# Optimization experiments

Hardware: AMD Instinct MI355X
Metric: run time of the kernel (lower is better)

Reference implementation:

```python
import jax, jax.numpy as jnp
import numpy as np

FS = 100.0
NPERSEG = 200
Q = 2
N_POINTS = 2
N_COEF = 2 * Q + 1          # bandstop doubles prototype order: len(a) = 2*Q + 1
EDGE = 3 * N_COEF           # scipy filtfilt default padlen = 3*max(len(a), len(b))

# ---- numpy filter design (== scipy.signal.butter(Q, [lo, hi], 'bandstop', fs=fs)) ----
def _butter_bandstop(N, low, high, fs):
    Wn = np.array([low, high]) / (fs / 2.0)
    fs2 = 2.0
    warped = 2.0 * fs2 * np.tan(np.pi * Wn / fs2)           # bilinear prewarp
    k = np.arange(1, N + 1)
    p = np.exp(1j * np.pi * (2 * k + N - 1) / (2 * N))      # analog Butterworth poles
    wo = np.sqrt(warped[0] * warped[1]); bw = warped[1] - warped[0]
    p_hp = (bw / 2.0) / p                                   # lp2bs_zpk
    p_bs = np.concatenate([p_hp + np.sqrt(p_hp ** 2 - wo ** 2), p_hp - np.sqrt(p_hp ** 2 - wo ** 2)])
    z_bs = np.concatenate([np.full(N, 1j * wo), np.full(N, -1j * wo)])
    k_bs = np.real(1.0 / np.prod(-p))
    fs2b = 2.0 * fs2                                        # bilinear_zpk
    z_z = (fs2b + z_bs) / (fs2b - z_bs)
    p_z = (fs2b + p_bs) / (fs2b - p_bs)
    k_z = k_bs * np.real(np.prod(fs2b - z_bs) / np.prod(fs2b - p_bs))
    b = np.real(k_z * np.poly(z_z)); a = np.real(np.poly(p_z))
    return b, a

def _lfilter_zi(b, a):
    n = len(a)
    A = np.zeros((n - 1, n - 1)); A[0, :] = -a[1:] / a[0]; A[1:, :-1] = np.eye(n - 2)
    B = b[1:] - a[1:] * b[0]
    return np.linalg.solve(np.eye(n - 1) - A.T, B)


def setup_inputs() -> dict:
    key = jax.random.key(0)
    B, T, H = 64, 3000, 256
    df = FS / NPERSEG
    f0 = np.arange(NPERSEG // 2 + 1) * df                   # welch freqs
    f0[0] = f0[1]; f0[-1] = f0[-2]
    col0, col1 = f0[:-1], f0[1:]
    freq_index = np.argsort(-col0, kind='stable')           # 'highest' strategy, descending
    high = float(col1[-1])
    lows = col0[freq_index[2:-1]]                           # 97 bandstop low edges
    bs, az, zs = [], [], []
    for lo in lows:
        b, a = _butter_bandstop(Q, float(lo), high, FS)
        bs.append(b); az.append(a); zs.append(_lfilter_zi(b, a))
    kx, kw1, kw2 = jax.random.split(key, 3)
    return {
        'x': jax.random.normal(kx, (B, T), jnp.float32),
        'b_all': jnp.asarray(np.stack(bs), jnp.float32),
        'a_all': jnp.asarray(np.stack(az), jnp.float32),
        'zi_all': jnp.asarray(np.stack(zs), jnp.float32),
        'W1': jax.random.normal(kw1, (T, H), jnp.float32) / np.sqrt(T),
        'b1': jnp.zeros((H,), jnp.float32),
        'w2': jax.random.normal(kw2, (H,), jnp.float32) / np.sqrt(H),
        'freq_index': jnp.asarray(freq_index, jnp.int32),
    }


# ---- batched zero-phase IIR filtering over the whole filter bank ----
def _lfilter(b, a, x, zi):
    # b, a: [F, n]; x: [F, B, T]; zi: [F, B, n-1]; direct-form II transposed
    b0 = b[:, 0][:, None]
    b_rest = b[:, 1:][:, None, :]
    a_rest = a[:, 1:][:, None, :]
    def step(z, xt):
        y = b0 * xt + z[..., 0]
        z_shift = jnp.concatenate([z[..., 1:], jnp.zeros_like(z[..., :1])], axis=-1)
        return z_shift + b_rest * xt[..., None] - a_rest * y[..., None], y
    _, ys = jax.lax.scan(step, zi, jnp.moveaxis(x, -1, 0))
    return jnp.moveaxis(ys, 0, -1)

def _filtfilt(b, a, zi, x):
    # odd extension by EDGE samples on both ends (scipy padtype='odd')
    left = 2.0 * x[..., :1] - jnp.flip(x[..., 1:EDGE + 1], -1)
    right = 2.0 * x[..., -1:] - jnp.flip(x[..., -EDGE - 1:-1], -1)
    ext = jnp.concatenate([left, x, right], -1)
    y = _lfilter(b, a, ext, zi[:, None, :] * ext[..., :1])
    y = jnp.flip(_lfilter(b, a, jnp.flip(y, -1), zi[:, None, :] * y[..., -1:]), -1)
    return y[..., EDGE:-EDGE]

def _fn(p, W1, b1, w2):
    # explained model: scalar score per sample (last axis is time/features)
    return jnp.tanh(p @ W1 + b1) @ w2


def reference(x, b_all, a_all, zi_all, W1, b1, w2, freq_index):
    F = b_all.shape[0]
    bs_out = _filtfilt(b_all, a_all, zi_all, jnp.broadcast_to(x, (F,) + x.shape))  # [97,B,T]
    # filter outputs in order: Identity, Identity, 97 bandstops, SpectralErase; x_all[0] = start point
    x_all = jnp.concatenate([x[None], x[None], x[None], bs_out, jnp.zeros_like(x)[None]], 0)  # [101,B,T]
    x_next, x_prev = x_all[1:], x_all[:-1]
    delta = x_prev - x_next                                   # x_i - x_i1 (path from x_i1 to x_i)
    alphas = jnp.linspace(0.0, 1.0, N_POINTS).astype(x.dtype)
    pts = x_next[None] + alphas[:, None, None, None] * delta[None]  # [n_points,100,B,T]
    g = jax.grad(lambda p: _fn(p, W1, b1, w2).sum())(pts)           # per-sample grads (fn is batched)
    grads = g.mean(0) * delta                                       # line integral, [100,B,T]
    out = jnp.moveaxis(grads, 0, -1)                                # [B,T,100]
    return out[:, :, freq_index]
```

## Files before the change

kernel.cpp:

```cpp
#include <hip/hip_runtime.h>
#include <math.h>

#define T_LEN 3000
#define NF 97
#define NB 64
#define NH 256
#define NI 100
#define SEQ 6336
#define KCO 16
#define KS 10
#define KPB 300
#define KC2 15
#define UPROWS 6400
#define LF 202
#define LB 201
#define NSEG 15
#define WTS 3072
#define VTS 6400

__device__ __forceinline__ void gload16(const float* g, float* l) {
    __builtin_amdgcn_global_load_lds(
        (const __attribute__((address_space(1))) void*)g,
        (__attribute__((address_space(3))) void*)l, 16, 0, 0);
}

__global__ __launch_bounds__(256) void k_prep(
    const float* __restrict__ x, float* __restrict__ Pt)
{
    const int kk0 = blockIdx.x * 64;
    const int b   = threadIdx.x & 63;
    const int ko  = threadIdx.x >> 6;
    #pragma unroll
    for (int p = 0; p < 16; ++p) {
        int kk = kk0 + ko + 4*p;
        if (kk < T_LEN) Pt[(size_t)kk*SEQ + b] = x[(size_t)b*T_LEN + kk];
    }
}

__global__ __launch_bounds__(256) void k_wt(
    const float* __restrict__ W1, float* __restrict__ W1T)
{
    __shared__ float tile[64][65];
    const int tb = blockIdx.x;
    const int hb = blockIdx.y;
    const int lt = threadIdx.x & 63, lw = threadIdx.x >> 6;
    #pragma unroll
    for (int i = 0; i < 16; ++i) {
        int t = tb*64 + lw*16 + i; if (t > T_LEN-1) t = T_LEN-1;
        tile[lw*16+i][lt] = W1[(size_t)t*NH + hb*64 + lt];
    }
    __syncthreads();
    #pragma unroll
    for (int i = 0; i < 16; ++i) {
        int h = hb*64 + lw*16 + i;
        W1T[(size_t)h*WTS + tb*64 + lt] = tile[lt][lw*16+i];
    }
}

__global__ __launch_bounds__(64) void k_hom(
    const float* __restrict__ a_all, double* __restrict__ H,
    double* __restrict__ Mbd, double* __restrict__ Mfd)
{
    const int ft = blockIdx.x*64 + threadIdx.x;
    const int f = ft >> 2, ib = ft & 3;
    if (f >= NF) return;
    const double a1 = a_all[f*5+1], a2 = a_all[f*5+2],
                 a3 = a_all[f*5+3], a4 = a_all[f*5+4];
    double z0 = (ib==0), z1 = (ib==1), z2 = (ib==2), z3 = (ib==3);
    for (int j = 0; j <= LF; ++j) {
        if (j < LF) H[((size_t)f*LF + j)*4 + ib] = z0;
        if (j == LB) {
            Mbd[f*16 + 0*4 + ib] = z0; Mbd[f*16 + 1*4 + ib] = z1;
            Mbd[f*16 + 2*4 + ib] = z2; Mbd[f*16 + 3*4 + ib] = z3;
        }
        if (j == LF) {
            Mfd[f*16 + 0*4 + ib] = z0; Mfd[f*16 + 1*4 + ib] = z1;
            Mfd[f*16 + 2*4 + ib] = z2; Mfd[f*16 + 3*4 + ib] = z3;
            break;
        }
        double yv = z0;
        z0 = z1 - a1*yv; z1 = z2 - a2*yv; z2 = z3 - a3*yv; z3 = -a4*yv;
    }
}

#define COEFS \
    const double bc0 = b_all[f*5+0], bc1 = b_all[f*5+1], bc2 = b_all[f*5+2], \
                 bc3 = b_all[f*5+3], bc4 = b_all[f*5+4]; \
    const double ac1 = a_all[f*5+1], ac2 = a_all[f*5+2], \
                 ac3 = a_all[f*5+3], ac4 = a_all[f*5+4];

#define FSTEP(XV, DST) { double xv = (XV); \
    double yv = fma(bc0, xv, z0); \
    z0 = fma(bc1, xv, z1) - ac1*yv; \
    z1 = fma(bc2, xv, z2) - ac2*yv; \
    z2 = fma(bc3, xv, z3) - ac3*yv; \
    z3 = bc4*xv - ac4*yv; \
    DST = (float)yv; }

__global__ __launch_bounds__(64) void k_seg_fwd(
    float* Pt, const float* __restrict__ b_all, const float* __restrict__ a_all,
    const float* __restrict__ zi_all, float* __restrict__ YRb,
    double* __restrict__ Zef)
{
    const int f = blockIdx.x, p = blockIdx.y, b = threadIdx.x;
    COEFS
    const float* xc = Pt + b;
    float* ycol = Pt + 64 + (size_t)f*64 + b;
    double z0 = 0, z1 = 0, z2 = 0, z3 = 0;

    if (p == 0) {
        const double x0 = (double)xc[0];
        const double e0 = 2.0*x0 - (double)xc[(size_t)15*SEQ];
        z0 = (double)zi_all[f*4+0]*e0; z1 = (double)zi_all[f*4+1]*e0;
        z2 = (double)zi_all[f*4+2]*e0; z3 = (double)zi_all[f*4+3]*e0;
        float le[15];
        #pragma unroll
        for (int i = 0; i < 15; ++i) le[i] = xc[(size_t)(15-i)*SEQ];
        #pragma unroll
        for (int i = 0; i < 15; ++i) { float o; FSTEP(2.0*x0 - (double)le[i], o); (void)o; }
    }
    int kk0, n;
    if (p == 0)       { kk0 = 0;          n = 187; }
    else if (p < 14)  { kk0 = p*LF - 15;  n = LF;  }
    else              { kk0 = 2813;       n = 187; }

    {
        const int nc = n/20, rem = n - nc*20;
        float A[20], B[20], C[20];
#define LDF(BUF, c) { _Pragma("unroll") \
        for (int j = 0; j < 20; ++j) BUF[j] = xc[(size_t)(kk0+(c)*20+j)*SEQ]; }
#define CHF(BUF, c) { _Pragma("unroll") \
        for (int j = 0; j < 20; ++j) { float o; FSTEP((double)BUF[j], o); \
            ycol[(size_t)(kk0+(c)*20+j)*SEQ] = o; } }
        if (nc > 0) LDF(A, 0); if (nc > 1) LDF(B, 1); if (nc > 2) LDF(C, 2);
        for (int g = 0; g < nc; g += 3) {
            CHF(A, g); if (g+3 < nc) LDF(A, g+3);
            if (g+1 < nc) { CHF(B, g+1); if (g+4 < nc) LDF(B, g+4); }
            if (g+2 < nc) { CHF(C, g+2); if (g+5 < nc) LDF(C, g+5); }
        }
        if (rem) {
            float T[19];
            #pragma unroll
            for (int j = 0; j < 19; ++j) if (j < rem) T[j] = xc[(size_t)(kk0+nc*20+j)*SEQ];
            #pragma unroll
            for (int j = 0; j < 19; ++j) if (j < rem) {
                float o; FSTEP((double)T[j], o); ycol[(size_t)(kk0+nc*20+j)*SEQ] = o;
            }
        }
#undef LDF
#undef CHF
    }
    if (p == 14) {
        const double xl = (double)xc[(size_t)(T_LEN-1)*SEQ];
        float re[15];
        #pragma unroll
        for (int i = 0; i < 15; ++i) re[i] = xc[(size_t)(2998-i)*SEQ];
        #pragma unroll
        for (int i = 0; i < 15; ++i) {
            float o; FSTEP(2.0*xl - (double)re[i], o);
            YRb[((size_t)f*15 + i)*64 + b] = o;
        }
    }
    double* ze = Zef + (((size_t)f*NSEG + p)*64 + b)*4;
    ze[0] = z0; ze[1] = z1; ze[2] = z2; ze[3] = z3;
}

__global__ __launch_bounds__(64) void k_stitch(
    const double* __restrict__ Ze, const double* __restrict__ Mm,
    double* __restrict__ Zo)
{
    const int f = blockIdx.x, b = threadIdx.x;
    double m[16];
    #pragma unroll
    for (int r = 0; r < 16; ++r) m[r] = Mm[f*16 + r];
    const double* z0p = Ze + (((size_t)f*NSEG + 0)*64 + b)*4;
    double z0 = z0p[0], z1 = z0p[1], z2 = z0p[2], z3 = z0p[3];
    {   double* o = Zo + (((size_t)f*NSEG + 1)*64 + b)*4;
        o[0]=z0; o[1]=z1; o[2]=z2; o[3]=z3; }
    for (int p = 1; p <= 13; ++p) {
        const double* zep = Ze + (((size_t)f*NSEG + p)*64 + b)*4;
        double n0 = zep[0] + m[0]*z0  + m[1]*z1  + m[2]*z2  + m[3]*z3;
        double n1 = zep[1] + m[4]*z0  + m[5]*z1  + m[6]*z2  + m[7]*z3;
        double n2 = zep[2] + m[8]*z0  + m[9]*z1  + m[10]*z2 + m[11]*z3;
        double n3 = zep[3] + m[12]*z0 + m[13]*z1 + m[14]*z2 + m[15]*z3;
        z0 = n0; z1 = n1; z2 = n2; z3 = n3;
        double* o = Zo + (((size_t)f*NSEG + p + 1)*64 + b)*4;
        o[0]=z0; o[1]=z1; o[2]=z2; o[3]=z3;
    }
}

__global__ __launch_bounds__(64) void k_corr_fwd(
    float* Pt, float* __restrict__ YRb, const double* __restrict__ H,
    const double* __restrict__ Zf)
{
    const int f = blockIdx.x, p = blockIdx.y + 1, b = threadIdx.x;
    const double* zp = Zf + (((size_t)f*NSEG + p)*64 + b)*4;
    const double w0 = zp[0], w1 = zp[1], w2 = zp[2], w3 = zp[3];
    const double* Hf = H + (size_t)f*LF*4;
    float* ycol = Pt + 64 + (size_t)f*64 + b;
    float* yrp  = YRb + (size_t)f*15*64 + b;
    const int s0 = p*LF;
    #pragma unroll 4
    for (int j = 0; j < LF; ++j) {
        const int s = s0 + j;
        double corr = Hf[j*4+0]*w0 + Hf[j*4+1]*w1 + Hf[j*4+2]*w2 + Hf[j*4+3]*w3;
        if (s < 3015) {
            float* d = &ycol[(size_t)(s-15)*SEQ];
            *d = (float)((double)*d + corr);
        } else {
            float* d = &yrp[(size_t)(s-3015)*64];
            *d = (float)((double)*d + corr);
        }
    }
}

__global__ __launch_bounds__(64) void k_seg_bwd(
    float* Pt, const float* __restrict__ b_all, const float* __restrict__ a_all,
    const float* __restrict__ zi_all, const float* __restrict__ YRb,
    double* __restrict__ Zeb)
{
    const int f = blockIdx.x, p = blockIdx.y, b = threadIdx.x;
    COEFS
    float* ycol = Pt + 64 + (size_t)f*64 + b;
    const float* yrp = YRb + (size_t)f*15*64 + b;
    double z0 = 0, z1 = 0, z2 = 0, z3 = 0;

    if (p == 0) {
        const double yl = (double)yrp[14*64];
        z0 = (double)zi_all[f*4+0]*yl; z1 = (double)zi_all[f*4+1]*yl;
        z2 = (double)zi_all[f*4+2]*yl; z3 = (double)zi_all[f*4+3]*yl;
        float t15[15];
        #pragma unroll
        for (int i = 0; i < 15; ++i) t15[i] = yrp[(size_t)(14-i)*64];
        #pragma unroll
        for (int i = 0; i < 15; ++i) { float o; FSTEP((double)t15[i], o); (void)o; }
    }
    int kkH, n;
    if (p == 0) { kkH = 2999; n = 186; }
    else        { kkH = 3014 - LB*p; n = LB; }

    {
        const int nc = n/20, rem = n - nc*20;
        float A[20], B[20], C[20];
#define LDBc(BUF, c) { _Pragma("unroll") \
        for (int j = 0; j < 20; ++j) BUF[j] = ycol[(size_t)(kkH-19-20*(c)+j)*SEQ]; }
#define CHBc(BUF, c) { _Pragma("unroll") \
        for (int j = 19; j >= 0; --j) { float o; FSTEP((double)BUF[j], o); BUF[j] = o; } \
        _Pragma("unroll") \
        for (int j = 0; j < 20; ++j) ycol[(size_t)(kkH-19-20*(c)+j)*SEQ] = BUF[j]; }
        if (nc > 0) LDBc(A, 0); if (nc > 1) LDBc(B, 1); if (nc > 2) LDBc(C, 2);
        for (int g = 0; g < nc; g += 3) {
            CHBc(A, g); if (g+3 < nc) LDBc(A, g+3);
            if (g+1 < nc) { CHBc(B, g+1); if (g+4 < nc) LDBc(B, g+4); }
            if (g+2 < nc) { CHBc(C, g+2); if (g+5 < nc) LDBc(C, g+5); }
        }
        if (rem) {
            float T[19];
            #pragma unroll
            for (int j = 0; j < 19; ++j) if (j < rem) T[j] = ycol[(size_t)(kkH-20*nc-j)*SEQ];
            #pragma unroll
            for (int j = 0; j < 19; ++j) if (j < rem) {
                float o; FSTEP((double)T[j], o); ycol[(size_t)(kkH-20*nc-j)*SEQ] = o;
            }
        }
#undef LDBc
#undef CHBc
    }
    double* ze = Zeb + (((size_t)f*NSEG + p)*64 + b)*4;
    ze[0] = z0; ze[1] = z1; ze[2] = z2; ze[3] = z3;
}

__global__ __launch_bounds__(64) void k_corr_bwd(
    float* Pt, const double* __restrict__ H, const double* __restrict__ Zb)
{
    const int f = blockIdx.x, p = blockIdx.y + 1, b = threadIdx.x;
    const double* zp = Zb + (((size_t)f*NSEG + p)*64 + b)*4;
    const double w0 = zp[0], w1 = zp[1], w2 = zp[2], w3 = zp[3];
    const double* Hf = H + (size_t)f*LF*4;
    float* ycol = Pt + 64 + (size_t)f*64 + b;
    const int q0 = p*LB;
    #pragma unroll 4
    for (int j = 0; j < LB; ++j) {
        const int kk = 3014 - (q0 + j);
        double corr = Hf[j*4+0]*w0 + Hf[j*4+1]*w1 + Hf[j*4+2]*w2 + Hf[j*4+3]*w3;
        float* d = &ycol[(size_t)kk*SEQ];
        *d = (float)((double)*d + corr);
    }
}
#undef FSTEP
#undef COEFS

__global__ __launch_bounds__(256) void k_ugemm(
    const float* __restrict__ Pt, const float* __restrict__ W1,
    float* __restrict__ Up)
{
    __shared__ float As[2][16*128];
    __shared__ float Bs[2][16*128];
    const int tid = threadIdx.x;
    const int rq = blockIdx.x, hq = blockIdx.y, ks = blockIdx.z;
    const int r0 = rq*128, h0 = hq*128;
    const int tg = tid & 15, ig = tid >> 4;
    const int wv = tid >> 6, lane = tid & 63;
    const int rowoff = lane >> 5;
    int colA = r0 + (lane & 31)*4; if (colA > SEQ-4) colA = SEQ-4;
    const int colB = h0 + (lane & 31)*4;

    float acc[8][8] = {};

#define STAGE_UG(cc, bf) { \
        const int k0s = ks*KPB + (cc)*KC2; \
        _Pragma("unroll") \
        for (int q = 0; q < 2; ++q) { \
            int j = wv + 4*q; \
            int r = 2*j + rowoff; if (r > 14) r = 14; \
            gload16(Pt + (size_t)(k0s+r)*SEQ + colA, &As[bf][j*256]); \
            gload16(W1 + (size_t)(k0s+r)*NH + colB, &Bs[bf][j*256]); \
        } }

    STAGE_UG(0, 0);
    __syncthreads();
    int cur = 0;
    for (int c = 0; c < KPB/KC2; ++c) {
        if (c + 1 < KPB/KC2) STAGE_UG(c + 1, cur ^ 1);
        #pragma unroll 5
        for (int k = 0; k < KC2; ++k) {
            float4 alo = *(const float4*)&As[cur][k*128 + tg*4];
            float4 ahi = *(const float4*)&As[cur][k*128 + 64 + tg*4];
            float4 blo = *(const float4*)&Bs[cur][k*128 + ig*4];
            float4 bhi = *(const float4*)&Bs[cur][k*128 + 64 + ig*4];
            float a[8] = {alo.x,alo.y,alo.z,alo.w,ahi.x,ahi.y,ahi.z,ahi.w};
            float b[8] = {blo.x,blo.y,blo.z,blo.w,bhi.x,bhi.y,bhi.z,bhi.w};
            #pragma unroll
            for (int mt = 0; mt < 8; ++mt)
                #pragma unroll
                for (int nn = 0; nn < 8; ++nn)
                    acc[mt][nn] = fmaf(a[mt], b[nn], acc[mt][nn]);
        }
        __syncthreads();
        cur ^= 1;
    }
#undef STAGE_UG

    float* up = Up + (size_t)ks*UPROWS*NH;
    #pragma unroll
    for (int mt = 0; mt < 8; ++mt) {
        const int r = r0 + (mt>>2)*64 + tg*4 + (mt&3);
        if (r < SEQ) {
            *(float4*)&up[(size_t)r*NH + h0 + ig*4]
                = make_float4(acc[mt][0], acc[mt][1], acc[mt][2], acc[mt][3]);
            *(float4*)&up[(size_t)r*NH + h0 + 64 + ig*4]
                = make_float4(acc[mt][4], acc[mt][5], acc[mt][6], acc[mt][7]);
        }
    }
}

__global__ __launch_bounds__(256) void k_uvred(
    const float* __restrict__ Up, const float* __restrict__ b1,
    const float* __restrict__ w2, const int* __restrict__ freq_index,
    float* __restrict__ Vt)
{
    __shared__ float Vtile[32][257];
    const int n0 = blockIdx.x * 32;
    const int h  = threadIdx.x;
    const float b1v = b1[h], w2v = w2[h];
    const float thp = tanhf(b1v);
    const float upseudo = (1.f - thp*thp) * w2v;
    for (int r = 0; r < 32; ++r) {
        int np = n0 + r;
        int bb = np / 100, jj = np - bb*100;
        int ii = freq_index[jj];
        int ra = (ii <= 2) ? bb : 64 + (ii-3)*64 + bb;
        float sa = Up[(size_t)ra*NH + h];
        #pragma unroll
        for (int ks = 1; ks < KS; ++ks)
            sa += Up[(size_t)ks*UPROWS*NH + (size_t)ra*NH + h];
        float ta = tanhf(sa + b1v);
        float ua = (1.f - ta*ta) * w2v;
        float ub;
        if (ii >= 99) ub = upseudo;
        else {
            int rb = (ii <= 1) ? bb : 64 + (ii-2)*64 + bb;
            float sb = Up[(size_t)rb*NH + h];
            #pragma unroll
            for (int ks = 1; ks < KS; ++ks)
                sb += Up[(size_t)ks*UPROWS*NH + (size_t)rb*NH + h];
            float tb_ = tanhf(sb + b1v);
            ub = (1.f - tb_*tb_) * w2v;
        }
        Vtile[r][h] = 0.5f*(ua + ub);
    }
    __syncthreads();
    const int ln = threadIdx.x & 31;
    const int hg = threadIdx.x >> 5;
    for (int m = 0; m < 32; ++m) {
        int hh = hg*32 + m;
        Vt[(size_t)hh*VTS + n0 + ln] = Vtile[ln][hh];
    }
}

__global__ __launch_bounds__(256) void k_delta(
    const float* __restrict__ Pt, const int* __restrict__ freq_index,
    float* __restrict__ out)
{
    __shared__ float Lv[99*65];
    __shared__ int fx[NI];
    const int t   = blockIdx.x;
    const int tid = threadIdx.x;
    if (tid < NI) fx[tid] = freq_index[tid];
    const float* ptrow = Pt + (size_t)t*SEQ;
    for (int c4 = tid; c4 < SEQ/4; c4 += 256) {
        float4 v = *(const float4*)(ptrow + c4*4);
        const int j  = c4 >> 4;
        const int bb = (c4 & 15) << 2;
        float* dst = &Lv[j*65 + bb];
        dst[0] = v.x; dst[1] = v.y; dst[2] = v.z; dst[3] = v.w;
    }
    __syncthreads();
    for (int q = tid; q < 1600; q += 256) {
        const int bb = q / 25, f4 = q - bb*25;
        float v[4];
        #pragma unroll
        for (int k = 0; k < 4; ++k) {
            const int ii = fx[f4*4 + k];
            const int ja = (ii <= 2) ? 0 : (ii - 2);
            float rv = Lv[ja*65 + bb];
            float rvn;
            if (ii >= 99) rvn = 0.f;
            else {
                const int jb = (ii <= 1) ? 0 : (ii - 1);
                rvn = Lv[jb*65 + bb];
            }
            v[k] = rv - rvn;
        }
        *(float4*)&out[(size_t)bb*T_LEN*NI + (size_t)t*NI + f4*4]
            = make_float4(v[0], v[1], v[2], v[3]);
    }
}

__global__ __launch_bounds__(256) void k_out(
    const float* __restrict__ W1T, const float* __restrict__ Vt,
    float* __restrict__ out)
{
    __shared__ float As[2][16*128];
    __shared__ float Vs[2][16*128];
    const int tid = threadIdx.x;
    const int tb  = blockIdx.x;
    const int nb  = blockIdx.y;

    const int tg = tid & 15;
    const int ig = tid >> 4;
    const int t0 = tb*128, n0 = nb*128;
    const int wv = tid >> 6, lane = tid & 63;
    const int rowoff = lane >> 5;
    const int coloff = (lane & 31)*4;

    const int npA = n0 + ig*4;
    const int bbA = npA / 100, jjA = npA - bbA*100;
    const int npB = npA + 64;
    const int bbB = npB / 100, jjB = npB - bbB*100;

    float acc[8][8] = {};

#define STAGE_KO(cc, bf) { \
        const int k0s = (cc)*KCO; \
        _Pragma("unroll") \
        for (int q = 0; q < 2; ++q) { \
            int j = wv + 4*q; \
            int r = 2*j + rowoff; \
            gload16(W1T + (size_t)(k0s+r)*WTS + t0 + coloff, &As[bf][j*256]); \
            gload16(Vt  + (size_t)(k0s+r)*VTS + n0 + coloff, &Vs[bf][j*256]); \
        } }

    STAGE_KO(0, 0);
    __syncthreads();
    int cur = 0;
    for (int c = 0; c < 16; ++c) {
        if (c + 1 < 16) STAGE_KO(c + 1, cur ^ 1);
        #pragma unroll 4
        for (int k = 0; k < KCO; ++k) {
            float4 alo = *(const float4*)&As[cur][k*128 + tg*4];
            float4 ahi = *(const float4*)&As[cur][k*128 + 64 + tg*4];
            float4 vlo = *(const float4*)&Vs[cur][k*128 + ig*4];
            float4 vhi = *(const float4*)&Vs[cur][k*128 + 64 + ig*4];
            float a[8] = {alo.x, alo.y, alo.z, alo.w, ahi.x, ahi.y, ahi.z, ahi.w};
            float v[8] = {vlo.x, vlo.y, vlo.z, vlo.w, vhi.x, vhi.y, vhi.z, vhi.w};
            #pragma unroll
            for (int mt = 0; mt < 8; ++mt)
                #pragma unroll
                for (int nn = 0; nn < 8; ++nn)
                    acc[mt][nn] = fmaf(a[mt], v[nn], acc[mt][nn]);
        }
        __syncthreads();
        cur ^= 1;
    }
#undef STAGE_KO

    #pragma unroll
    for (int mt = 0; mt < 8; ++mt) {
        const int t = t0 + (mt>>2)*64 + tg*4 + (mt&3);
        if (t < T_LEN) {
            float* oA = &out[(size_t)bbA*T_LEN*NI + (size_t)t*NI + jjA];
            float4 dA = *(const float4*)oA;
            *(float4*)oA = make_float4(acc[mt][0]*dA.x, acc[mt][1]*dA.y,
                                       acc[mt][2]*dA.z, acc[mt][3]*dA.w);
            float* oB = &out[(size_t)bbB*T_LEN*NI + (size_t)t*NI + jjB];
            float4 dB = *(const float4*)oB;
            *(float4*)oB = make_float4(acc[mt][4]*dB.x, acc[mt][5]*dB.y,
                                       acc[mt][6]*dB.z, acc[mt][7]*dB.w);
        }
    }
}

extern "C" void kernel_launch(void* const* d_in, const int* in_sizes, int n_in,
                              void* d_out, int out_size, void* d_ws, size_t ws_size,
                              hipStream_t stream) {
    const float* x      = (const float*)d_in[0];
    const float* b_all  = (const float*)d_in[1];
    const float* a_all  = (const float*)d_in[2];
    const float* zi_all = (const float*)d_in[3];
    const float* W1     = (const float*)d_in[4];
    const float* b1     = (const float*)d_in[5];
    const float* w2     = (const float*)d_in[6];
    const int*   fidx   = (const int*)d_in[7];
    float* out = (float*)d_out;

    float* Pt  = (float*)d_ws;
    float* Vt  = Pt + (size_t)T_LEN * SEQ;
    float* W1T = Vt + (size_t)NH * VTS;

    double* Hd  = (double*)d_out;
    double* Mfd = Hd + (size_t)NF*LF*4;
    double* Mbd = Mfd + NF*16;
    double* Zef = Mbd + NF*16;
    double* Zeb = Zef + (size_t)NF*NSEG*64*4;
    double* Zfd = Zeb + (size_t)NF*NSEG*64*4;
    double* Zbd = Zfd + (size_t)NF*NSEG*64*4;
    float*  YRb = (float*)(Zbd + (size_t)NF*NSEG*64*4);
    float*  Up  = out;

    hipLaunchKernelGGL(k_prep, dim3((T_LEN+63)/64), dim3(256), 0, stream,
                       x, Pt);
    hipLaunchKernelGGL(k_wt, dim3(WTS/64, NH/64), dim3(256), 0, stream,
                       W1, W1T);
    hipLaunchKernelGGL(k_hom, dim3(7), dim3(64), 0, stream,
                       a_all, Hd, Mbd, Mfd);
    hipLaunchKernelGGL(k_seg_fwd, dim3(NF, NSEG), dim3(64), 0, stream,
                       Pt, b_all, a_all, zi_all, YRb, Zef);
    hipLaunchKernelGGL(k_stitch, dim3(NF), dim3(64), 0, stream,
                       Zef, Mfd, Zfd);
    hipLaunchKernelGGL(k_corr_fwd, dim3(NF, 14), dim3(64), 0, stream,
                       Pt, YRb, Hd, Zfd);
    hipLaunchKernelGGL(k_seg_bwd, dim3(NF, NSEG), dim3(64), 0, stream,
                       Pt, b_all, a_all, zi_all, YRb, Zeb);
    hipLaunchKernelGGL(k_stitch, dim3(NF), dim3(64), 0, stream,
                       Zeb, Mbd, Zbd);
    hipLaunchKernelGGL(k_corr_bwd, dim3(NF, 14), dim3(64), 0, stream,
                       Pt, Hd, Zbd);
    hipLaunchKernelGGL(k_ugemm, dim3(50, 2, KS), dim3(256), 0, stream,
                       Pt, W1, Up);
    hipLaunchKernelGGL(k_uvred, dim3(UPROWS/32), dim3(256), 0, stream,
                       Up, b1, w2, fidx, Vt);
    hipLaunchKernelGGL(k_delta, dim3(T_LEN), dim3(256), 0, stream,
                       Pt, fidx, out);
    hipLaunchKernelGGL(k_out, dim3((T_LEN+127)/128, (NB*NI)/128), dim3(256), 0, stream,
                       W1T, Vt, out);
}
```

Baseline: 515.3 us.

## Fuse forward correction into backward segment pass and merge init kernels

Merges the transpose, W1 transpose and homogeneous-response kernels into one launch. Removes the separate forward-correction kernel by applying the forward stitch correction on the fly while loading values in the backward segment filter. To make that possible, the backward segments are realigned to the forward segment length, so a single homogeneous matrix serves both directions. This saves two launches and one read-modify-write pass over the filtered buffer, at the cost of extra FLOPs inside the serial backward kernel.

```diff
diff --git a/kernel.cpp b/kernel.cpp
--- a/kernel.cpp
+++ b/kernel.cpp
@@ -13,7 +13,6 @@
 #define KC2 15
 #define UPROWS 6400
 #define LF 202
-#define LB 201
 #define NSEG 15
 #define WTS 3072
 #define VTS 6400
@@ -24,62 +23,56 @@
         (__attribute__((address_space(3))) void*)l, 16, 0, 0);
 }
 
-__global__ __launch_bounds__(256) void k_prep(
-    const float* __restrict__ x, float* __restrict__ Pt)
-{
-    const int kk0 = blockIdx.x * 64;
-    const int b   = threadIdx.x & 63;
-    const int ko  = threadIdx.x >> 6;
-    #pragma unroll
-    for (int p = 0; p < 16; ++p) {
-        int kk = kk0 + ko + 4*p;
-        if (kk < T_LEN) Pt[(size_t)kk*SEQ + b] = x[(size_t)b*T_LEN + kk];
-    }
-}
-
-__global__ __launch_bounds__(256) void k_wt(
-    const float* __restrict__ W1, float* __restrict__ W1T)
-{
-    __shared__ float tile[64][65];
-    const int tb = blockIdx.x;
-    const int hb = blockIdx.y;
-    const int lt = threadIdx.x & 63, lw = threadIdx.x >> 6;
-    #pragma unroll
-    for (int i = 0; i < 16; ++i) {
-        int t = tb*64 + lw*16 + i; if (t > T_LEN-1) t = T_LEN-1;
-        tile[lw*16+i][lt] = W1[(size_t)t*NH + hb*64 + lt];
-    }
-    __syncthreads();
-    #pragma unroll
-    for (int i = 0; i < 16; ++i) {
-        int h = hb*64 + lw*16 + i;
-        W1T[(size_t)h*WTS + tb*64 + lt] = tile[lt][lw*16+i];
-    }
-}
-
-__global__ __launch_bounds__(64) void k_hom(
-    const float* __restrict__ a_all, double* __restrict__ H,
-    double* __restrict__ Mbd, double* __restrict__ Mfd)
-{
-    const int ft = blockIdx.x*64 + threadIdx.x;
-    const int f = ft >> 2, ib = ft & 3;
-    if (f >= NF) return;
-    const double a1 = a_all[f*5+1], a2 = a_all[f*5+2],
-                 a3 = a_all[f*5+3], a4 = a_all[f*5+4];
-    double z0 = (ib==0), z1 = (ib==1), z2 = (ib==2), z3 = (ib==3);
-    for (int j = 0; j <= LF; ++j) {
-        if (j < LF) H[((size_t)f*LF + j)*4 + ib] = z0;
-        if (j == LB) {
-            Mbd[f*16 + 0*4 + ib] = z0; Mbd[f*16 + 1*4 + ib] = z1;
-            Mbd[f*16 + 2*4 + ib] = z2; Mbd[f*16 + 3*4 + ib] = z3;
-        }
-        if (j == LF) {
-            Mfd[f*16 + 0*4 + ib] = z0; Mfd[f*16 + 1*4 + ib] = z1;
-            Mfd[f*16 + 2*4 + ib] = z2; Mfd[f*16 + 3*4 + ib] = z3;
-            break;
-        }
-        double yv = z0;
-        z0 = z1 - a1*yv; z1 = z2 - a2*yv; z2 = z3 - a3*yv; z3 = -a4*yv;
+__global__ __launch_bounds__(256) void k_init(
+    const float* __restrict__ x, const float* __restrict__ W1,
+    const float* __restrict__ a_all, float* __restrict__ Pt,
+    float* __restrict__ W1T, double* __restrict__ H, double* __restrict__ Mfd)
+{
+    const int blk = blockIdx.x;
+    if (blk < 47) {
+        const int kk0 = blk * 64;
+        const int b   = threadIdx.x & 63;
+        const int ko  = threadIdx.x >> 6;
+        #pragma unroll
+        for (int p = 0; p < 16; ++p) {
+            int kk = kk0 + ko + 4*p;
+            if (kk < T_LEN) Pt[(size_t)kk*SEQ + b] = x[(size_t)b*T_LEN + kk];
+        }
+    } else if (blk < 239) {
+        __shared__ float tile[64][65];
+        const int w  = blk - 47;
+        const int tb = w & 47 ? w % 48 : w % 48;
+        const int hb = w / 48;
+        const int lt = threadIdx.x & 63, lw = threadIdx.x >> 6;
+        #pragma unroll
+        for (int i = 0; i < 16; ++i) {
+            int t = tb*64 + lw*16 + i; if (t > T_LEN-1) t = T_LEN-1;
+            tile[lw*16+i][lt] = W1[(size_t)t*NH + hb*64 + lt];
+        }
+        __syncthreads();
+        #pragma unroll
+        for (int i = 0; i < 16; ++i) {
+            int h = hb*64 + lw*16 + i;
+            W1T[(size_t)h*WTS + tb*64 + lt] = tile[lt][lw*16+i];
+        }
+    } else {
+        if (threadIdx.x >= 64) return;
+        const int ft = (blk - 239)*64 + threadIdx.x;
+        const int f = ft >> 2, ib = ft & 3;
+        if (f >= NF) return;
+        const double a1 = a_all[f*5+1], a2 = a_all[f*5+2],
+                     a3 = a_all[f*5+3], a4 = a_all[f*5+4];
+        double z0 = (ib==0), z1 = (ib==1), z2 = (ib==2), z3 = (ib==3);
+        for (int j = 0; j <= LF; ++j) {
+            if (j < LF) H[((size_t)f*LF + j)*4 + ib] = z0;
+            if (j == LF) {
+                Mfd[f*16 + 0*4 + ib] = z0; Mfd[f*16 + 1*4 + ib] = z1;
+                Mfd[f*16 + 2*4 + ib] = z2; Mfd[f*16 + 3*4 + ib] = z3;
+                break;
+            }
+            double yv = z0;
+            z0 = z1 - a1*yv; z1 = z2 - a2*yv; z2 = z3 - a3*yv; z3 = -a4*yv;
+        }
     }
 }
 
@@ -189,61 +182,50 @@
     }
 }
 
-__global__ __launch_bounds__(64) void k_corr_fwd(
-    float* Pt, float* __restrict__ YRb, const double* __restrict__ H,
-    const double* __restrict__ Zf)
-{
-    const int f = blockIdx.x, p = blockIdx.y + 1, b = threadIdx.x;
-    const double* zp = Zf + (((size_t)f*NSEG + p)*64 + b)*4;
-    const double w0 = zp[0], w1 = zp[1], w2 = zp[2], w3 = zp[3];
-    const double* Hf = H + (size_t)f*LF*4;
-    float* ycol = Pt + 64 + (size_t)f*64 + b;
-    float* yrp  = YRb + (size_t)f*15*64 + b;
-    const int s0 = p*LF;
-    #pragma unroll 4
-    for (int j = 0; j < LF; ++j) {
-        const int s = s0 + j;
-        double corr = Hf[j*4+0]*w0 + Hf[j*4+1]*w1 + Hf[j*4+2]*w2 + Hf[j*4+3]*w3;
-        if (s < 3015) {
-            float* d = &ycol[(size_t)(s-15)*SEQ];
-            *d = (float)((double)*d + corr);
-        } else {
-            float* d = &yrp[(size_t)(s-3015)*64];
-            *d = (float)((double)*d + corr);
-        }
-    }
-}
-
 __global__ __launch_bounds__(64) void k_seg_bwd(
     float* Pt, const float* __restrict__ b_all, const float* __restrict__ a_all,
     const float* __restrict__ zi_all, const float* __restrict__ YRb,
+    const double* __restrict__ H, const double* __restrict__ Zf,
     double* __restrict__ Zeb)
 {
-    const int f = blockIdx.x, p = blockIdx.y, b = threadIdx.x;
+    const int f = blockIdx.x, bq = blockIdx.y, b = threadIdx.x;
     COEFS
+    const int q = 14 - bq;
     float* ycol = Pt + 64 + (size_t)f*64 + b;
     const float* yrp = YRb + (size_t)f*15*64 + b;
+    const double* Hf = H + (size_t)f*LF*4;
+    double w0 = 0, w1 = 0, w2 = 0, w3 = 0;
+    if (q >= 1) {
+        const double* zp = Zf + (((size_t)f*NSEG + q)*64 + b)*4;
+        w0 = zp[0]; w1 = zp[1]; w2 = zp[2]; w3 = zp[3];
+    }
     double z0 = 0, z1 = 0, z2 = 0, z3 = 0;
 
-    if (p == 0) {
-        const double yl = (double)yrp[14*64];
+#define CORR(J) (Hf[(J)*4+0]*w0 + Hf[(J)*4+1]*w1 + Hf[(J)*4+2]*w2 + Hf[(J)*4+3]*w3)
+
+    if (bq == 0) {
+        const float ylf = (float)((double)yrp[14*64] + CORR(201));
+        const double yl = (double)ylf;
         z0 = (double)zi_all[f*4+0]*yl; z1 = (double)zi_all[f*4+1]*yl;
         z2 = (double)zi_all[f*4+2]*yl; z3 = (double)zi_all[f*4+3]*yl;
         float t15[15];
         #pragma unroll
-        for (int i = 0; i < 15; ++i) t15[i] = yrp[(size_t)(14-i)*64];
+        for (int i = 0; i < 15; ++i)
+            t15[i] = (float)((double)yrp[(size_t)(14-i)*64] + CORR(201-i));
         #pragma unroll
         for (int i = 0; i < 15; ++i) { float o; FSTEP((double)t15[i], o); (void)o; }
     }
-    int kkH, n;
-    if (p == 0) { kkH = 2999; n = 186; }
-    else        { kkH = 3014 - LB*p; n = LB; }
+    const int kkH  = (bq == 0) ? 2999 : 202*q + 186;
+    const int n    = (bq == 0 || bq == 14) ? 187 : 202;
+    const int joff = 15 - 202*q;
 
     {
         const int nc = n/20, rem = n - nc*20;
         float A[20], B[20], C[20];
 #define LDBc(BUF, c) { _Pragma("unroll") \
-        for (int j = 0; j < 20; ++j) BUF[j] = ycol[(size_t)(kkH-19-20*(c)+j)*SEQ]; }
+        for (int j = 0; j < 20; ++j) { \
+            const int kk = kkH-19-20*(c)+j; \
+            BUF[j] = (float)((double)ycol[(size_t)kk*SEQ] + CORR(kk + joff)); } }
 #define CHBc(BUF, c) { _Pragma("unroll") \
         for (int j = 19; j >= 0; --j) { float o; FSTEP((double)BUF[j], o); BUF[j] = o; } \
         _Pragma("unroll") \
@@ -257,7 +239,10 @@
         if (rem) {
             float T[19];
             #pragma unroll
-            for (int j = 0; j < 19; ++j) if (j < rem) T[j] = ycol[(size_t)(kkH-20*nc-j)*SEQ];
+            for (int j = 0; j < 19; ++j) if (j < rem) {
+                const int kk = kkH - 20*nc - j;
+                T[j] = (float)((double)ycol[(size_t)kk*SEQ] + CORR(kk + joff));
+            }
             #pragma unroll
             for (int j = 0; j < 19; ++j) if (j < rem) {
                 float o; FSTEP((double)T[j], o); ycol[(size_t)(kkH-20*nc-j)*SEQ] = o;
@@ -266,23 +251,26 @@
 #undef LDBc
 #undef CHBc
     }
-    double* ze = Zeb + (((size_t)f*NSEG + p)*64 + b)*4;
+#undef CORR
+    double* ze = Zeb + (((size_t)f*NSEG + bq)*64 + b)*4;
     ze[0] = z0; ze[1] = z1; ze[2] = z2; ze[3] = z3;
 }
 
 __global__ __launch_bounds__(64) void k_corr_bwd(
     float* Pt, const double* __restrict__ H, const double* __restrict__ Zb)
 {
-    const int f = blockIdx.x, p = blockIdx.y + 1, b = threadIdx.x;
-    const double* zp = Zb + (((size_t)f*NSEG + p)*64 + b)*4;
+    const int f = blockIdx.x, bq = blockIdx.y + 1, b = threadIdx.x;
+    const int q = 14 - bq;
+    const double* zp = Zb + (((size_t)f*NSEG + bq)*64 + b)*4;
     const double w0 = zp[0], w1 = zp[1], w2 = zp[2], w3 = zp[3];
     const double* Hf = H + (size_t)f*LF*4;
     float* ycol = Pt + 64 + (size_t)f*64 + b;
-    const int q0 = p*LB;
+    const int kk_top = (bq < 14) ? 202*q + 186 : 186;
+    const int n      = (bq < 14) ? 202 : 187;
     #pragma unroll 4
-    for (int j = 0; j < LB; ++j) {
-        const int kk = 3014 - (q0 + j);
-        double corr = Hf[j*4+0]*w0 + Hf[j*4+1]*w1 + Hf[j*4+2]*w2 + Hf[j*4+3]*w3;
+    for (int jb = 0; jb < n; ++jb) {
+        const int kk = kk_top - jb;
+        double corr = Hf[jb*4+0]*w0 + Hf[jb*4+1]*w1 + Hf[jb*4+2]*w2 + Hf[jb*4+3]*w3;
         float* d = &ycol[(size_t)kk*SEQ];
         *d = (float)((double)*d + corr);
     }
@@ -530,30 +518,23 @@
 
     double* Hd  = (double*)d_out;
     double* Mfd = Hd + (size_t)NF*LF*4;
-    double* Mbd = Mfd + NF*16;
-    double* Zef = Mbd + NF*16;
+    double* Zef = Mfd + NF*16;
     double* Zeb = Zef + (size_t)NF*NSEG*64*4;
     double* Zfd = Zeb + (size_t)NF*NSEG*64*4;
     double* Zbd = Zfd + (size_t)NF*NSEG*64*4;
     float*  YRb = (float*)(Zbd + (size_t)NF*NSEG*64*4);
     float*  Up  = out;
 
-    hipLaunchKernelGGL(k_prep, dim3((T_LEN+63)/64), dim3(256), 0, stream,
-                       x, Pt);
-    hipLaunchKernelGGL(k_wt, dim3(WTS/64, NH/64), dim3(256), 0, stream,
-                       W1, W1T);
-    hipLaunchKernelGGL(k_hom, dim3(7), dim3(64), 0, stream,
-                       a_all, Hd, Mbd, Mfd);
+    hipLaunchKernelGGL(k_init, dim3(246), dim3(256), 0, stream,
+                       x, W1, a_all, Pt, W1T, Hd, Mfd);
     hipLaunchKernelGGL(k_seg_fwd, dim3(NF, NSEG), dim3(64), 0, stream,
                        Pt, b_all, a_all, zi_all, YRb, Zef);
     hipLaunchKernelGGL(k_stitch, dim3(NF), dim3(64), 0, stream,
                        Zef, Mfd, Zfd);
-    hipLaunchKernelGGL(k_corr_fwd, dim3(NF, 14), dim3(64), 0, stream,
-                       Pt, YRb, Hd, Zfd);
     hipLaunchKernelGGL(k_seg_bwd, dim3(NF, NSEG), dim3(64), 0, stream,
-                       Pt, b_all, a_all, zi_all, YRb, Zeb);
+                       Pt, b_all, a_all, zi_all, YRb, Hd, Zfd, Zeb);
     hipLaunchKernelGGL(k_stitch, dim3(NF), dim3(64), 0, stream,
-                       Zeb, Mbd, Zbd);
+                       Zeb, Mfd, Zbd);
     hipLaunchKernelGGL(k_corr_bwd, dim3(NF, 14), dim3(64), 0, stream,
                        Pt, Hd, Zbd);
     hipLaunchKernelGGL(k_ugemm, dim3(50, 2, KS), dim3(256), 0, stream,
```

Measured after the change: 430.8 us. -16.4%, faster.
